# Optimization experiments

Measured on AMD Instinct MI355X. Metric: run time of the kernel, lower is better.

The kernel has to match this reference:

```python
import jax, jax.numpy as jnp
import numpy as np

B = 8192
EPS = 1e-5  # BatchNorm eps (torch default)


def binarize(x):
    # sign binarization with straight-through estimator (matches the .data trick
    # in BinarizeConv2d/BinarizeLinear: forward sees +-1, backward sees identity)
    s = jnp.where(x >= 0, 1.0, -1.0).astype(x.dtype)
    return x + jax.lax.stop_gradient(s - x)


def conv2d(x, w, stride, pad):
    return jax.lax.conv_general_dilated(
        x, w, window_strides=stride, padding=pad,
        dimension_numbers=('NCHW', 'OIHW', 'NCHW'))


def bn(x, g, b, m, v):
    # eval-mode BatchNorm2d folded into one scale+shift per channel
    inv = g * jax.lax.rsqrt(v + EPS)
    return x * inv[None, :, None, None] + (b - m * inv)[None, :, None, None]


def maxpool_w2(x):
    # MaxPool2d(kernel=(1,2), stride=(1,2))
    return jax.lax.reduce_window(x, -jnp.inf, jax.lax.max,
                                 (1, 1, 1, 2), (1, 1, 1, 2), 'VALID')


def setup_inputs() -> dict:
    key = jax.random.key(0)
    ks = jax.random.split(key, 32)
    d = {}
    d['x'] = jax.random.normal(ks[0], (B, 1, 6, 128), jnp.float32)

    def w(k, shape):
        return jax.random.normal(k, shape, jnp.float32) * 0.05

    # conv weights (OIHW) and biases
    d['w1'] = w(ks[1], (32, 1, 1, 9));    d['b1'] = w(ks[2], (32,))
    d['w2'] = w(ks[3], (64, 32, 1, 3));   d['b2'] = w(ks[4], (64,))
    d['w3'] = w(ks[5], (128, 64, 1, 3));  d['b3'] = w(ks[6], (128,))
    d['w4'] = w(ks[7], (128, 128, 6, 1)); d['b4'] = w(ks[8], (128,))
    # BatchNorm params (gamma, beta, running_mean, running_var)
    for i, c in zip((1, 2, 3, 4), (32, 64, 128, 128)):
        kk = jax.random.split(ks[8 + i], 4)
        d[f'g{i}'] = 1.0 + 0.1 * jax.random.normal(kk[0], (c,), jnp.float32)
        d[f'be{i}'] = 0.1 * jax.random.normal(kk[1], (c,), jnp.float32)
        d[f'm{i}'] = 0.1 * jax.random.normal(kk[2], (c,), jnp.float32)
        d[f'v{i}'] = jax.random.uniform(kk[3], (c,), jnp.float32, 0.5, 1.5)
    # fc: BinarizeLinear(2048, 10)
    d['wf'] = w(ks[20], (10, 2048))
    d['bf'] = w(ks[21], (10,))
    return d


def reference(x, w1, b1, w2, b2, w3, b3, w4, b4,
              g1, be1, m1, v1, g2, be2, m2, v2,
              g3, be3, m3, v3, g4, be4, m4, v4, wf, bf):
    # block 1: first layer keeps real-valued input, binarized weights
    h = conv2d(x, binarize(w1), (1, 2), [(0, 0), (4, 4)]) + b1[None, :, None, None]
    h = jnp.clip(bn(h, g1, be1, m1, v1), -1.0, 1.0)   # Hardtanh
    h = maxpool_w2(h)                                  # [B,32,6,32]
    # block 2: binarized activations + weights
    h = conv2d(binarize(h), binarize(w2), (1, 1), [(0, 0), (1, 1)]) + b2[None, :, None, None]
    h = jnp.clip(bn(h, g2, be2, m2, v2), -1.0, 1.0)    # [B,64,6,32]
    # block 3
    h = conv2d(binarize(h), binarize(w3), (1, 1), [(0, 0), (1, 1)]) + b3[None, :, None, None]
    h = jnp.clip(bn(h, g3, be3, m3, v3), -1.0, 1.0)
    h = maxpool_w2(h)                                  # [B,128,6,16]
    # block 4: (6,1) kernel collapses H
    h = conv2d(binarize(h), binarize(w4), (1, 1), [(0, 0), (0, 0)]) + b4[None, :, None, None]
    h = jnp.clip(bn(h, g4, be4, m4, v4), -1.0, 1.0)    # [B,128,1,16]
    h = h.reshape(h.shape[0], -1)                      # [B,2048]
    return binarize(h) @ binarize(wf).T + bf           # [B,10]
```

## Files before the change

kernel.cpp:

```cpp
#include <hip/hip_runtime.h>
#include <cstdint>
#include <cstddef>

#define BN_EPS 1e-5f
#define BATCH 8192

typedef unsigned long long u64;
typedef uint32_t u32;
typedef int v4i __attribute__((ext_vector_type(4)));
typedef int v16i __attribute__((ext_vector_type(16)));

__device__ __forceinline__ u32 f2k(float f) {
    u32 u = __float_as_uint(f);
    return (u >> 31) ? ~u : (u | 0x80000000u);
}
__device__ __forceinline__ float k2f(u32 k) {
    u32 u = (k & 0x80000000u) ? (k ^ 0x80000000u) : ~k;
    return __uint_as_float(u);
}
__device__ __forceinline__ float bn_eval(float conv, float B, float iv, float sh) {
    return __fadd_rn(__fmul_rn(__fadd_rn(conv, B), iv), sh);
}

__global__ __launch_bounds__(256) void prep_all(
    const float* w1, const float* b1, const float* w2, const float* b2,
    const float* w3, const float* b3, const float* w4, const float* b4,
    const float* wf,
    const float* g1, const float* be1, const float* m1, const float* v1,
    const float* g2, const float* be2, const float* m2, const float* v2,
    const float* g3, const float* be3, const float* m3, const float* v3,
    const float* g4, const float* be4, const float* m4, const float* v4,
    float* s1, float* T1, u32* wt2w, int* T2,
    uint4* b3i8, int* C3, u64* wt4, int* T4, u64* wtf) {
    int t = blockIdx.x * 256 + threadIdx.x;

    if (t < 288) {
        int co = t / 9;
        float iv = g1[co] * rsqrtf(v1[co] + BN_EPS);
        float d = (iv < 0.f) ? -1.f : 1.f;
        s1[t] = ((w1[t] >= 0.f) ? 1.f : -1.f) * d;
    } else if (t < 320) {
        int co = t - 288;
        float iv = g1[co] * rsqrtf(v1[co] + BN_EPS);
        float sh = be1[co] - m1[co] * iv;
        float B = b1[co];
        bool flip = (iv < 0.f);
        auto pred = [&](float sp) {
            float sum = flip ? -sp : sp;
            return bn_eval(sum, B, iv, sh) >= 0.f;
        };
        u32 lo = f2k(-3.0e38f), hi = f2k(3.0e38f);
        float Tv;
        if (pred(k2f(lo))) Tv = k2f(lo);
        else if (!pred(k2f(hi))) Tv = __uint_as_float(0x7F800000u);
        else {
            while (hi - lo > 1u) {
                u32 mid = lo + ((hi - lo) >> 1);
                if (pred(k2f(mid))) hi = mid; else lo = mid;
            }
            Tv = k2f(hi);
        }
        T1[co] = Tv;
    } else if (t < 512) {
        int idx = t - 320;
        int co = idx / 3, kw = idx % 3;
        float iv = g2[co] * rsqrtf(v2[co] + BN_EPS);
        bool flip = (iv < 0.f);
        u32 wb = 0;
        for (int ci = 0; ci < 32; ++ci)
            wb |= (u32)((w2[(co * 32 + ci) * 3 + kw] >= 0.f) != flip) << ci;
        wt2w[co * 4 + kw] = wb;
    } else if (t < 704) {
        int idx = t - 512;
        int co = idx & 63, cls = idx >> 6;
        float iv = g2[co] * rsqrtf(v2[co] + BN_EPS);
        float sh = be2[co] - m2[co] * iv;
        float B = b2[co];
        bool flip = (iv < 0.f);
        int spur = 0, nv = 3;
        if (cls == 1) { nv = 2; for (int ci = 0; ci < 32; ++ci) spur += (int)((w2[(co * 32 + ci) * 3 + 0] >= 0.f) != flip); }
        if (cls == 2) { nv = 2; for (int ci = 0; ci < 32; ++ci) spur += (int)((w2[(co * 32 + ci) * 3 + 2] >= 0.f) != flip); }
        int maxp = 32 * nv + spur;
        int T = -1;
        for (int p = 0; p <= maxp; ++p) {
            int conv = flip ? (2 * (p - spur) - 32 * nv) : (32 * nv - 2 * (p - spur));
            float y = bn_eval((float)conv, B, iv, sh);
            if ((y >= 0.f) && (T == p - 1)) T = p;
        }
        T2[cls * 64 + co] = T;
    } else if (t < 2240) {
        int idx = t - 704;
        int q = idx >> 7, n = idx & 127;
        float iv = g3[n] * rsqrtf(v3[n] + BN_EPS);
        bool flip = (iv < 0.f);
        int kw = q >> 2, ci0 = (q & 3) * 16;
        u32 wd[4] = {0, 0, 0, 0};
        for (int j = 0; j < 16; ++j) {
            int ci = ci0 + j;
            bool pos = (w3[(n * 64 + ci) * 3 + kw] >= 0.f) != flip;
            u32 byte = pos ? 0x01u : 0xFFu;
            wd[j >> 2] |= byte << (8 * (j & 3));
        }
        b3i8[idx] = make_uint4(wd[0], wd[1], wd[2], wd[3]);
    } else if (t < 2368) {
        int co = t - 2240;
        float iv = g3[co] * rsqrtf(v3[co] + BN_EPS);
        float sh = be3[co] - m3[co] * iv;
        float B = b3[co];
        int C = 1000;
        if (iv >= 0.f) {
            for (int v = -192; v <= 192; v += 2)
                if (bn_eval((float)v, B, iv, sh) >= 0.f) { C = v; break; }
        } else {
            for (int v = 192; v >= -192; v -= 2)
                if (bn_eval((float)v, B, iv, sh) >= 0.f) { C = -v; break; }
        }
        C3[co] = C;
    } else if (t < 3904) {
        int idx = t - 2368;
        int j = idx & 1, ch = idx >> 1;
        int co = ch / 6, h = ch % 6;
        float iv = g4[co] * rsqrtf(v4[co] + BN_EPS);
        bool flip = (iv < 0.f);
        u64 wb = 0;
        for (int cb = 0; cb < 64; ++cb) {
            int ci = j * 64 + cb;
            wb |= (u64)((w4[(co * 128 + ci) * 6 + h] >= 0.f) != flip) << cb;
        }
        wt4[idx] = wb;
    } else if (t < 4032) {
        int co = t - 3904;
        float iv = g4[co] * rsqrtf(v4[co] + BN_EPS);
        float sh = be4[co] - m4[co] * iv;
        float B = b4[co];
        bool flip = (iv < 0.f);
        int T = -1;
        for (int p = 0; p <= 768; ++p) {
            int conv = flip ? (2 * p - 768) : (768 - 2 * p);
            float y = bn_eval((float)conv, B, iv, sh);
            if ((y >= 0.f) && (T == p - 1)) T = p;
        }
        T4[co] = T;
    } else if (t < 4352) {
        int idx = t - 4032;
        int o = idx / 32, wi = idx % 32;
        u64 wb = 0;
        for (int fb = 0; fb < 64; ++fb)
            wb |= (u64)(wf[o * 2048 + wi * 64 + fb] >= 0.f) << fb;
        wtf[idx] = wb;
    }
}

__global__ __launch_bounds__(256) void layer1_kernel(
    const float* __restrict__ x, const float* __restrict__ s1, const float* __restrict__ T1,
    u32* __restrict__ a1) {
    __shared__ float sS[288], sT[32];
    int t = threadIdx.x;
    for (int i = t; i < 288; i += 256) sS[i] = s1[i];
    if (t < 32) sT[t] = T1[t];
    __syncthreads();
    int gid = blockIdx.x * 256 + t;
    int wp = gid & 31;
    int bh = gid >> 5;
    const float* xp = x + (size_t)bh * 128;
    float xv[11];
    int p0 = 4 * wp - 4;
#pragma unroll
    for (int j = 0; j < 11; ++j) {
        int p = p0 + j;
        xv[j] = (p >= 0 && p < 128) ? xp[p] : 0.f;
    }
    u32 word = 0;
#pragma unroll
    for (int co = 0; co < 32; ++co) {
        float sum0 = 0.f, sum1 = 0.f;
#pragma unroll
        for (int k = 0; k < 9; ++k) {
            float wv = sS[co * 9 + k];
            sum0 = fmaf(wv, xv[k], sum0);
            sum1 = fmaf(wv, xv[k + 2], sum1);
        }
        float Tt = sT[co];
        word |= (u32)((sum0 >= Tt) || (sum1 >= Tt)) << co;
    }
    a1[gid] = word;
}

__global__ __launch_bounds__(256) void layer2_kernel(
    const u32* __restrict__ a1, const uint4* __restrict__ wt2v, const int* __restrict__ T2,
    u64* __restrict__ a2) {
    __shared__ uint4 sW[64];
    __shared__ int sT[192];
    int t = threadIdx.x;
    if (t < 64) sW[t] = wt2v[t];
    if (t < 192) sT[t] = T2[t];
    __syncthreads();
    int gid = blockIdx.x * 256 + t;
    int w = gid & 31;
    int bh = gid >> 5;
    const u32* ap = a1 + (size_t)bh * 32;
    u32 am = ap[w];
    u32 al = (w > 0) ? ap[w - 1] : 0u;
    u32 ar = (w < 31) ? ap[w + 1] : 0u;
    const int* Tp = &sT[(w == 0) ? 64 : ((w == 31) ? 128 : 0)];
    u64 word = 0;
#pragma unroll
    for (int co = 0; co < 64; ++co) {
        uint4 wv = sW[co];
        int p = __popc(al ^ wv.x) + __popc(am ^ wv.y) + __popc(ar ^ wv.z);
        word |= (u64)(p <= Tp[co]) << co;
    }
    a2[gid] = word;
}

#define L3_ROWS 8
__global__ __launch_bounds__(256) void layer3_mfma(
    const u64* __restrict__ a2, const uint4* __restrict__ b3i8, const int* __restrict__ C3,
    u32* __restrict__ a3u32) {
    __shared__ uint4 sB[12 * 128];
    __shared__ u64 sLUT[256];
    __shared__ int sC3[128];
    int t = threadIdx.x;
    for (int i = t; i < 1536; i += 256) sB[i] = b3i8[i];
    {
        u32 b = t & 255;
        u64 e = 0;
#pragma unroll
        for (int j = 0; j < 8; ++j)
            e |= (((b >> j) & 1) ? 0x01ull : 0xFFull) << (8 * j);
        if (t < 256) sLUT[t] = e;
    }
    if (t < 128) sC3[t] = C3[t];
    __syncthreads();

    int wv = t >> 6, lane = t & 63, m = lane & 31, half = lane >> 5;
    int rowBase = (blockIdx.x * 4 + wv) * L3_ROWS;
    const int prTab[8] = {0, 1, 4, 5, 8, 9, 12, 13};

    for (int r = 0; r < L3_ROWS; ++r) {
        int bh = rowBase + r;
        u64 aw = a2[(size_t)bh * 32 + m];
        u64 wm1 = __shfl(aw, m - 1);
        u64 wp1 = __shfl(aw, m + 1);

        v4i A[6];
#pragma unroll
        for (int kk = 0; kk < 6; ++kk) {
            const int kw = kk >> 1;
            u64 word = (kw == 0) ? wm1 : ((kw == 1) ? aw : wp1);
            bool valid = !((kw == 0 && m == 0) || (kw == 2 && m == 31));
            int ci0 = ((kk & 1) << 5) + (half << 4);
            u32 bits = (u32)(word >> ci0) & 0xFFFFu;
            u64 lo = sLUT[bits & 0xFF];
            u64 hi = sLUT[bits >> 8];
            if (!valid) { lo = 0; hi = 0; }
            union { u64 q[2]; v4i v; } u;
            u.q[0] = lo; u.q[1] = hi;
            A[kk] = u.v;
        }

        u32 outv = 0;
#pragma unroll
        for (int nt = 0; nt < 4; ++nt) {
            v16i acc;
#pragma unroll
            for (int i = 0; i < 16; ++i) acc[i] = 0;
#pragma unroll
            for (int kk = 0; kk < 6; ++kk) {
                int q = kk * 2 + half;
                union { uint4 u4; v4i v; } bu;
                bu.u4 = sB[q * 128 + nt * 32 + m];
                acc = __builtin_amdgcn_mfma_i32_32x32x32_i8(A[kk], bu.v, acc, 0, 0, 0);
            }
            int tc = sC3[nt * 32 + m];
#pragma unroll
            for (int rp = 0; rp < 8; ++rp) {
                bool c = (acc[2 * rp] >= tc) || (acc[2 * rp + 1] >= tc);
                u64 mk = __ballot(c);
                int LA = (nt << 4) | prTab[rp];
                int LB = LA + 2;
                outv = (lane == LA) ? (u32)mk : outv;
                outv = (lane == LB) ? (u32)(mk >> 32) : outv;
            }
        }
        a3u32[(size_t)bh * 64 + ((lane & 15) << 2) + (lane >> 4)] = outv;
    }
}

__global__ __launch_bounds__(256) void layer4_fc_kernel(
    const u64* __restrict__ a3, const u64* __restrict__ wt4, const int* __restrict__ T4,
    const u64* __restrict__ wtf, const float* __restrict__ bf, float* __restrict__ out) {
    __shared__ u64 sW4[1536];
    __shared__ u64 sWf[320];
    __shared__ u64 sFeat[16][32];
    __shared__ int sT[128];
    __shared__ float sBf[10];
    int t = threadIdx.x;
    {
        ulonglong2* d = (ulonglong2*)sW4;
        const ulonglong2* s = (const ulonglong2*)wt4;
        for (int i = t; i < 768; i += 256) d[i] = s[i];
        ulonglong2* df = (ulonglong2*)sWf;
        const ulonglong2* sf = (const ulonglong2*)wtf;
        if (t < 160) df[t] = sf[t];
    }
    if (t < 128) sT[t] = T4[t];
    if (t < 10) sBf[t] = bf[t];
    __syncthreads();
    int bb = t >> 4, w = t & 15, lane = t & 63, g = lane >> 4;
    int b = blockIdx.x * 16 + bb;
    u64 av[12];
#pragma unroll
    for (int h = 0; h < 6; ++h) {
        av[h * 2 + 0] = a3[(size_t)b * 192 + h * 32 + w * 2 + 0];
        av[h * 2 + 1] = a3[(size_t)b * 192 + h * 32 + w * 2 + 1];
    }
    u64 acc = 0;
#pragma unroll 8
    for (int co = 0; co < 128; ++co) {
        const u64* wr = &sW4[co * 12];
        int p = 0;
#pragma unroll
        for (int q = 0; q < 12; ++q) p += __popcll(av[q] ^ wr[q]);
        u64 m = __ballot(p <= sT[co]);
        u64 field = (m >> (g * 16)) & 0xFFFFull;
        acc |= field << ((co & 3) << 4);
        if ((co & 3) == 3) {
            if (w == 0) sFeat[bb][co >> 2] = acc;
            acc = 0;
        }
    }
    __syncthreads();
    if (t < 160) {
        int fb = t / 10, o = t % 10;
        int p = 0;
#pragma unroll
        for (int wi = 0; wi < 32; ++wi) p += __popcll(sFeat[fb][wi] ^ sWf[o * 32 + wi]);
        out[(size_t)(blockIdx.x * 16 + fb) * 10 + o] = __fadd_rn((float)(2048 - 2 * p), sBf[o]);
    }
}

extern "C" void kernel_launch(void* const* d_in, const int* in_sizes, int n_in,
                              void* d_out, int out_size, void* d_ws, size_t ws_size,
                              hipStream_t stream) {
    const float* x  = (const float*)d_in[0];
    const float* w1 = (const float*)d_in[1];  const float* b1 = (const float*)d_in[2];
    const float* w2 = (const float*)d_in[3];  const float* b2 = (const float*)d_in[4];
    const float* w3 = (const float*)d_in[5];  const float* b3 = (const float*)d_in[6];
    const float* w4 = (const float*)d_in[7];  const float* b4 = (const float*)d_in[8];
    const float* g1 = (const float*)d_in[9];  const float* be1 = (const float*)d_in[10];
    const float* m1 = (const float*)d_in[11]; const float* v1 = (const float*)d_in[12];
    const float* g2 = (const float*)d_in[13]; const float* be2 = (const float*)d_in[14];
    const float* m2 = (const float*)d_in[15]; const float* v2 = (const float*)d_in[16];
    const float* g3 = (const float*)d_in[17]; const float* be3 = (const float*)d_in[18];
    const float* m3 = (const float*)d_in[19]; const float* v3 = (const float*)d_in[20];
    const float* g4 = (const float*)d_in[21]; const float* be4 = (const float*)d_in[22];
    const float* m4 = (const float*)d_in[23]; const float* v4 = (const float*)d_in[24];
    const float* wf = (const float*)d_in[25]; const float* bf = (const float*)d_in[26];
    float* out = (float*)d_out;

    char* ws = (char*)d_ws;
    u32* a1 = (u32*)(ws + 0);
    u64* a2 = (u64*)(ws + 6291456);
    u64* a3 = (u64*)(ws + 18874368);
    const size_t S = 31457280;
    uint4* b3i8 = (uint4*)(ws + S + 0);
    u64*  wt4  = (u64*) (ws + S + 24576);
    u64*  wtf  = (u64*) (ws + S + 36864);
    u32*  wt2w = (u32*) (ws + S + 39424);
    float* s1  = (float*)(ws + S + 40448);
    float* T1  = (float*)(ws + S + 41600);
    int*  T2   = (int*)  (ws + S + 41728);
    int*  C3   = (int*)  (ws + S + 42496);
    int*  T4   = (int*)  (ws + S + 43008);

    prep_all<<<17, 256, 0, stream>>>(w1, b1, w2, b2, w3, b3, w4, b4, wf,
                                     g1, be1, m1, v1, g2, be2, m2, v2,
                                     g3, be3, m3, v3, g4, be4, m4, v4,
                                     s1, T1, wt2w, T2, b3i8, C3, wt4, T4, wtf);

    layer1_kernel<<<(BATCH * 6 * 32) / 256, 256, 0, stream>>>(x, s1, T1, a1);
    layer2_kernel<<<(BATCH * 6 * 32) / 256, 256, 0, stream>>>(a1, (const uint4*)wt2w, T2, a2);
    layer3_mfma<<<(BATCH * 6) / (4 * L3_ROWS), 256, 0, stream>>>(a2, b3i8, C3, (u32*)a3);
    layer4_fc_kernel<<<BATCH / 16, 256, 0, stream>>>(a3, wt4, T4, wtf, bf, out);
}
```

Before: 277.2 us.

## Fuse layer1 and layer2 into one kernel via shared-memory activations

Merges the layer-1 conv and the layer-2 binary conv into a single kernel. Layer-1 bit words now stay in shared memory, so the a1 global buffer and one launch are gone. Layer-1 weights are padded to 12 per channel so they can be read as float4 from LDS. The layer3 L3_ROWS constant also drops from 8 to 4, which doubles its grid size and changes per-block work. The fused kernel adds a block barrier between the two stages.

```diff
diff --git a/kernel.cpp b/kernel.cpp
--- a/kernel.cpp
+++ b/kernel.cpp
@@ -30,17 +30,21 @@
     const float* g2, const float* be2, const float* m2, const float* v2,
     const float* g3, const float* be3, const float* m3, const float* v3,
     const float* g4, const float* be4, const float* m4, const float* v4,
-    float* s1, float* T1, u32* wt2w, int* T2,
+    float* s1f, float* T1, u32* wt2w, int* T2,
     uint4* b3i8, int* C3, u64* wt4, int* T4, u64* wtf) {
     int t = blockIdx.x * 256 + threadIdx.x;
 
-    if (t < 288) {
-        int co = t / 9;
-        float iv = g1[co] * rsqrtf(v1[co] + BN_EPS);
-        float d = (iv < 0.f) ? -1.f : 1.f;
-        s1[t] = ((w1[t] >= 0.f) ? 1.f : -1.f) * d;
-    } else if (t < 320) {
-        int co = t - 288;
+    if (t < 384) {
+        int co = t / 12, k = t % 12;
+        float val = 0.f;
+        if (k < 9) {
+            float iv = g1[co] * rsqrtf(v1[co] + BN_EPS);
+            float d = (iv < 0.f) ? -1.f : 1.f;
+            val = ((w1[co * 9 + k] >= 0.f) ? 1.f : -1.f) * d;
+        }
+        s1f[t] = val;
+    } else if (t < 416) {
+        int co = t - 384;
         float iv = g1[co] * rsqrtf(v1[co] + BN_EPS);
         float sh = be1[co] - m1[co] * iv;
         float B = b1[co];
@@ -61,8 +65,8 @@
             Tv = k2f(hi);
         }
         T1[co] = Tv;
-    } else if (t < 512) {
-        int idx = t - 320;
+    } else if (t < 608) {
+        int idx = t - 416;
         int co = idx / 3, kw = idx % 3;
         float iv = g2[co] * rsqrtf(v2[co] + BN_EPS);
         bool flip = (iv < 0.f);
@@ -70,8 +74,8 @@
         for (int ci = 0; ci < 32; ++ci)
             wb |= (u32)((w2[(co * 32 + ci) * 3 + kw] >= 0.f) != flip) << ci;
         wt2w[co * 4 + kw] = wb;
-    } else if (t < 704) {
-        int idx = t - 512;
+    } else if (t < 800) {
+        int idx = t - 608;
         int co = idx & 63, cls = idx >> 6;
         float iv = g2[co] * rsqrtf(v2[co] + BN_EPS);
         float sh = be2[co] - m2[co] * iv;
@@ -88,8 +92,8 @@
             if ((y >= 0.f) && (T == p - 1)) T = p;
         }
         T2[cls * 64 + co] = T;
-    } else if (t < 2240) {
-        int idx = t - 704;
+    } else if (t < 2336) {
+        int idx = t - 800;
         int q = idx >> 7, n = idx & 127;
         float iv = g3[n] * rsqrtf(v3[n] + BN_EPS);
         bool flip = (iv < 0.f);
@@ -102,8 +106,8 @@
             wd[j >> 2] |= byte << (8 * (j & 3));
         }
         b3i8[idx] = make_uint4(wd[0], wd[1], wd[2], wd[3]);
-    } else if (t < 2368) {
-        int co = t - 2240;
+    } else if (t < 2464) {
+        int co = t - 2336;
         float iv = g3[co] * rsqrtf(v3[co] + BN_EPS);
         float sh = be3[co] - m3[co] * iv;
         float B = b3[co];
@@ -116,8 +120,8 @@
                 if (bn_eval((float)v, B, iv, sh) >= 0.f) { C = -v; break; }
         }
         C3[co] = C;
-    } else if (t < 3904) {
-        int idx = t - 2368;
+    } else if (t < 4000) {
+        int idx = t - 2464;
         int j = idx & 1, ch = idx >> 1;
         int co = ch / 6, h = ch % 6;
         float iv = g4[co] * rsqrtf(v4[co] + BN_EPS);
@@ -128,8 +132,8 @@
             wb |= (u64)((w4[(co * 128 + ci) * 6 + h] >= 0.f) != flip) << cb;
         }
         wt4[idx] = wb;
-    } else if (t < 4032) {
-        int co = t - 3904;
+    } else if (t < 4128) {
+        int co = t - 4000;
         float iv = g4[co] * rsqrtf(v4[co] + BN_EPS);
         float sh = be4[co] - m4[co] * iv;
         float B = b4[co];
@@ -141,8 +145,8 @@
             if ((y >= 0.f) && (T == p - 1)) T = p;
         }
         T4[co] = T;
-    } else if (t < 4352) {
-        int idx = t - 4032;
+    } else if (t < 4448) {
+        int idx = t - 4128;
         int o = idx / 32, wi = idx % 32;
         u64 wb = 0;
         for (int fb = 0; fb < 64; ++fb)
@@ -151,17 +155,24 @@
     }
 }
 
-__global__ __launch_bounds__(256) void layer1_kernel(
-    const float* __restrict__ x, const float* __restrict__ s1, const float* __restrict__ T1,
-    u32* __restrict__ a1) {
-    __shared__ float sS[288], sT[32];
+#define L12_ROWS 8
+__global__ __launch_bounds__(256) void layer12_kernel(
+    const float* __restrict__ x, const float4* __restrict__ s1p, const float* __restrict__ T1,
+    const uint4* __restrict__ wt2v, const int* __restrict__ T2, u64* __restrict__ a2) {
+    __shared__ float4 sS[96];
+    __shared__ float sT[32];
+    __shared__ uint4 sW[64];
+    __shared__ int sT2[192];
+    __shared__ u32 sA1[L12_ROWS][32];
     int t = threadIdx.x;
-    for (int i = t; i < 288; i += 256) sS[i] = s1[i];
+    if (t < 96) sS[t] = s1p[t];
     if (t < 32) sT[t] = T1[t];
-    __syncthreads();
-    int gid = blockIdx.x * 256 + t;
-    int wp = gid & 31;
-    int bh = gid >> 5;
+    if (t < 64) sW[t] = wt2v[t];
+    if (t < 192) sT2[t] = T2[t];
+    __syncthreads();
+
+    int r = t >> 5, wp = t & 31;
+    int bh = blockIdx.x * L12_ROWS + r;
     const float* xp = x + (size_t)bh * 128;
     float xv[11];
     int p0 = 4 * wp - 4;
@@ -173,47 +184,40 @@
     u32 word = 0;
 #pragma unroll
     for (int co = 0; co < 32; ++co) {
+        float4 wa = sS[co * 3 + 0];
+        float4 wb = sS[co * 3 + 1];
+        float wc = sS[co * 3 + 2].x;
         float sum0 = 0.f, sum1 = 0.f;
-#pragma unroll
-        for (int k = 0; k < 9; ++k) {
-            float wv = sS[co * 9 + k];
-            sum0 = fmaf(wv, xv[k], sum0);
-            sum1 = fmaf(wv, xv[k + 2], sum1);
-        }
+        sum0 = fmaf(wa.x, xv[0], sum0);  sum1 = fmaf(wa.x, xv[2], sum1);
+        sum0 = fmaf(wa.y, xv[1], sum0);  sum1 = fmaf(wa.y, xv[3], sum1);
+        sum0 = fmaf(wa.z, xv[2], sum0);  sum1 = fmaf(wa.z, xv[4], sum1);
+        sum0 = fmaf(wa.w, xv[3], sum0);  sum1 = fmaf(wa.w, xv[5], sum1);
+        sum0 = fmaf(wb.x, xv[4], sum0);  sum1 = fmaf(wb.x, xv[6], sum1);
+        sum0 = fmaf(wb.y, xv[5], sum0);  sum1 = fmaf(wb.y, xv[7], sum1);
+        sum0 = fmaf(wb.z, xv[6], sum0);  sum1 = fmaf(wb.z, xv[8], sum1);
+        sum0 = fmaf(wb.w, xv[7], sum0);  sum1 = fmaf(wb.w, xv[9], sum1);
+        sum0 = fmaf(wc,   xv[8], sum0);  sum1 = fmaf(wc,   xv[10], sum1);
         float Tt = sT[co];
         word |= (u32)((sum0 >= Tt) || (sum1 >= Tt)) << co;
     }
-    a1[gid] = word;
-}
-
-__global__ __launch_bounds__(256) void layer2_kernel(
-    const u32* __restrict__ a1, const uint4* __restrict__ wt2v, const int* __restrict__ T2,
-    u64* __restrict__ a2) {
-    __shared__ uint4 sW[64];
-    __shared__ int sT[192];
-    int t = threadIdx.x;
-    if (t < 64) sW[t] = wt2v[t];
-    if (t < 192) sT[t] = T2[t];
-    __syncthreads();
-    int gid = blockIdx.x * 256 + t;
-    int w = gid & 31;
-    int bh = gid >> 5;
-    const u32* ap = a1 + (size_t)bh * 32;
-    u32 am = ap[w];
-    u32 al = (w > 0) ? ap[w - 1] : 0u;
-    u32 ar = (w < 31) ? ap[w + 1] : 0u;
-    const int* Tp = &sT[(w == 0) ? 64 : ((w == 31) ? 128 : 0)];
-    u64 word = 0;
+    sA1[r][wp] = word;
+    __syncthreads();
+
+    u32 am = sA1[r][wp];
+    u32 al = (wp > 0) ? sA1[r][wp - 1] : 0u;
+    u32 ar = (wp < 31) ? sA1[r][wp + 1] : 0u;
+    const int* Tp = &sT2[(wp == 0) ? 64 : ((wp == 31) ? 128 : 0)];
+    u64 word2 = 0;
 #pragma unroll
     for (int co = 0; co < 64; ++co) {
         uint4 wv = sW[co];
         int p = __popc(al ^ wv.x) + __popc(am ^ wv.y) + __popc(ar ^ wv.z);
-        word |= (u64)(p <= Tp[co]) << co;
-    }
-    a2[gid] = word;
-}
-
-#define L3_ROWS 8
+        word2 |= (u64)(p <= Tp[co]) << co;
+    }
+    a2[(size_t)bh * 32 + wp] = word2;
+}
+
+#define L3_ROWS 4
 __global__ __launch_bounds__(256) void layer3_mfma(
     const u64* __restrict__ a2, const uint4* __restrict__ b3i8, const int* __restrict__ C3,
     u32* __restrict__ a3u32) {
@@ -360,27 +364,26 @@
     float* out = (float*)d_out;
 
     char* ws = (char*)d_ws;
-    u32* a1 = (u32*)(ws + 0);
-    u64* a2 = (u64*)(ws + 6291456);
-    u64* a3 = (u64*)(ws + 18874368);
-    const size_t S = 31457280;
+    u64* a2 = (u64*)(ws + 0);
+    u64* a3 = (u64*)(ws + 12582912);
+    const size_t S = 25165824;
     uint4* b3i8 = (uint4*)(ws + S + 0);
     u64*  wt4  = (u64*) (ws + S + 24576);
     u64*  wtf  = (u64*) (ws + S + 36864);
     u32*  wt2w = (u32*) (ws + S + 39424);
-    float* s1  = (float*)(ws + S + 40448);
-    float* T1  = (float*)(ws + S + 41600);
-    int*  T2   = (int*)  (ws + S + 41728);
-    int*  C3   = (int*)  (ws + S + 42496);
-    int*  T4   = (int*)  (ws + S + 43008);
-
-    prep_all<<<17, 256, 0, stream>>>(w1, b1, w2, b2, w3, b3, w4, b4, wf,
+    float* s1f = (float*)(ws + S + 40448);
+    float* T1  = (float*)(ws + S + 41984);
+    int*  T2   = (int*)  (ws + S + 42112);
+    int*  C3   = (int*)  (ws + S + 42880);
+    int*  T4   = (int*)  (ws + S + 43392);
+
+    prep_all<<<18, 256, 0, stream>>>(w1, b1, w2, b2, w3, b3, w4, b4, wf,
                                      g1, be1, m1, v1, g2, be2, m2, v2,
                                      g3, be3, m3, v3, g4, be4, m4, v4,
-                                     s1, T1, wt2w, T2, b3i8, C3, wt4, T4, wtf);
-
-    layer1_kernel<<<(BATCH * 6 * 32) / 256, 256, 0, stream>>>(x, s1, T1, a1);
-    layer2_kernel<<<(BATCH * 6 * 32) / 256, 256, 0, stream>>>(a1, (const uint4*)wt2w, T2, a2);
+                                     s1f, T1, wt2w, T2, b3i8, C3, wt4, T4, wtf);
+
+    layer12_kernel<<<(BATCH * 6) / L12_ROWS, 256, 0, stream>>>(
+        x, (const float4*)s1f, T1, (const uint4*)wt2w, T2, a2);
     layer3_mfma<<<(BATCH * 6) / (4 * L3_ROWS), 256, 0, stream>>>(a2, b3i8, C3, (u32*)a3);
     layer4_fc_kernel<<<BATCH / 16, 256, 0, stream>>>(a3, wt4, T4, wtf, bf, out);
 }
```

After: 283.8 us. 2.4% more time.
